# Performance work log

Hardware: AMD Instinct MI355X
Metric: run time of the kernel (lower is better)

## Reference

```python
import jax, jax.numpy as jnp
import numpy as np

N_EMBD = 1024
N_HEAD = 16
HEAD_DIM = N_EMBD // N_HEAD


def setup_inputs() -> dict:
    key = jax.random.key(0)
    ks = jax.random.split(key, 5)
    B, S = 2, 2048
    scale = 0.02
    return {
        "hidden_states": jax.random.normal(ks[0], (B, S, N_EMBD), dtype=jnp.float32),
        "w_attn": jax.random.normal(ks[1], (N_EMBD, 3 * N_EMBD), dtype=jnp.float32) * scale,
        "b_attn": jnp.zeros((3 * N_EMBD,), dtype=jnp.float32),
        "w_proj": jax.random.normal(ks[2], (N_EMBD, N_EMBD), dtype=jnp.float32) * scale,
        "b_proj": jnp.zeros((N_EMBD,), dtype=jnp.float32),
    }


def reference(hidden_states, w_attn, b_attn, w_proj, b_proj):
    B, S, _ = hidden_states.shape
    qkv = hidden_states @ w_attn + b_attn                     # [B,S,3E]
    q, k, v = jnp.split(qkv, 3, axis=-1)                      # each [B,S,E]

    def split_heads(t):  # [B,S,E] -> [B,H,S,D]
        return t.reshape(B, S, N_HEAD, HEAD_DIM).transpose(0, 2, 1, 3)

    q, k, v = split_heads(q), split_heads(k), split_heads(v)

    scores = jnp.einsum("bhqd,bhkd->bhqk", q, k) / np.sqrt(HEAD_DIM).astype(np.float32)
    causal = jnp.tril(jnp.ones((S, S), dtype=bool))
    scores = jnp.where(causal[None, None], scores, jnp.float32(-jnp.inf))
    attn = jax.nn.softmax(scores, axis=-1)                    # [B,H,S,S]
    out = jnp.einsum("bhqk,bhkd->bhqd", attn, v)              # [B,H,S,D]
    out = out.transpose(0, 2, 1, 3).reshape(B, S, N_EMBD)     # merge heads
    out = out @ w_proj + b_proj
    return out
```

## Files before the change

### kernel.cpp

```cpp
#include <hip/hip_runtime.h>
#include <hip/hip_bf16.h>


typedef __attribute__((ext_vector_type(4))) float  float4v;
typedef __attribute__((ext_vector_type(8))) short  short8v;
typedef __attribute__((ext_vector_type(4))) short  short4v;

#define ATT_SCALE 0.18033688011112042f

__device__ __forceinline__ short f2bf(float f) {
  union { float f; unsigned u; } v; v.f = f;
  unsigned r = v.u + 0x7fffu + ((v.u >> 16) & 1u);
  return (short)(r >> 16);
}
__device__ __forceinline__ float bf2f(short s) {
  union { unsigned u; float f; } v; v.u = ((unsigned)(unsigned short)s) << 16;
  return v.f;
}

__device__ __forceinline__ short4v pack_bf16x4(float a, float b, float c, float d) {
  unsigned x0 = __builtin_bit_cast(unsigned, a) + 0x8000u;
  unsigned x1 = __builtin_bit_cast(unsigned, b) + 0x8000u;
  unsigned x2 = __builtin_bit_cast(unsigned, c) + 0x8000u;
  unsigned x3 = __builtin_bit_cast(unsigned, d) + 0x8000u;
  union { unsigned u[2]; short4v s; } r;
  r.u[0] = __builtin_amdgcn_perm(x1, x0, 0x07060302);
  r.u[1] = __builtin_amdgcn_perm(x3, x2, 0x07060302);
  return r.s;
}

__device__ __forceinline__ short4v cvt_pk_bf16x4(float a, float b, float c, float d) {
  union { unsigned u[2]; short4v s; } r;
  asm("v_cvt_pk_bf16_f32 %0, %1, %2" : "=v"(r.u[0]) : "v"(a), "v"(b));
  asm("v_cvt_pk_bf16_f32 %0, %1, %2" : "=v"(r.u[1]) : "v"(c), "v"(d));
  return r.s;
}

__device__ __forceinline__ void gl_lds16(const void* g, void* l) {
  __builtin_amdgcn_global_load_lds(
      (const __attribute__((address_space(1))) unsigned*)g,
      (__attribute__((address_space(3))) unsigned*)l, 16, 0, 0);
}

__global__ __launch_bounds__(256) void prep_kernel(
    const float* __restrict__ hidden, const float* __restrict__ w_attn,
    const float* __restrict__ w_proj, short* __restrict__ hA,
    short* __restrict__ wqkvT, short* __restrict__ wprojT) {
  __shared__ float tile[32][33];
  const int bx = blockIdx.x, t = threadIdx.x;
  if (bx < 4096) {
    const size_t i = ((size_t)bx * 256 + t) * 4;
    float4v v = *(const float4v*)(hidden + i);
    short4v o;
    #pragma unroll
    for (int k = 0; k < 4; k++) o[k] = f2bf(v[k]);
    *(short4v*)(hA + i) = o;
    return;
  }
  const float* in; short* out; int R, C, cx, cy;
  if (bx < 4096 + 3072) {
    in = w_attn; out = wqkvT; R = 1024; C = 3072;
    cx = (bx - 4096) % 96; cy = (bx - 4096) / 96;
  } else {
    in = w_proj; out = wprojT; R = 1024; C = 1024;
    cx = (bx - 7168) % 32; cy = (bx - 7168) / 32;
  }
  const int tx = t & 31, ty = t >> 5;
  const int c0 = cx * 32, r0 = cy * 32;
  #pragma unroll
  for (int i = 0; i < 4; i++)
    tile[ty + i * 8][tx] = in[(size_t)(r0 + ty + i * 8) * C + c0 + tx];
  __syncthreads();
  #pragma unroll
  for (int i = 0; i < 4; i++) {
    const int cc = ty + i * 8;
    out[(size_t)(c0 + cc) * R + r0 + tx] = f2bf(tile[tx][cc]);
  }
}

__global__ __launch_bounds__(512, 2) void gemm_qkv256(
    const short* __restrict__ A, const short* __restrict__ Bt,
    const float* __restrict__ bias, short* __restrict__ qkv,
    short* __restrict__ vA)
{
  __shared__ short As[2][256][64];
  __shared__ short Bs[2][256][64];
  const int K = 1024;
  const int t = threadIdx.x;
  const int lane = t & 63, w = t >> 6;
  const int wm2 = w >> 2, wn4 = w & 3;
  const int l16 = lane & 15, quad = lane >> 4;
  const int e7 = l16 & 7;
  const int row0 = blockIdx.y * 256;
  const int col0 = blockIdx.x * 256;

  float4v acc[8][4] = {};

  const int srow = w * 8 + (lane >> 3);
  const int slog = (lane & 7) ^ (lane >> 3);
  const short* gA = A + (size_t)(row0 + srow) * K + slog * 8;
  const short* gB = Bt + (size_t)(col0 + srow) * K + slog * 8;
  const int sdst = (lane & 7) * 8;

  auto stageA = [&](int b, int qd, int kt) {
    gl_lds16(gA + (size_t)qd * 64 * K + kt * 64,
             &As[b][qd * 64 + w * 8 + (lane >> 3)][sdst]);
  };
  auto stageB = [&](int b, int qd, int kt) {
    gl_lds16(gB + (size_t)qd * 64 * K + kt * 64,
             &Bs[b][qd * 64 + w * 8 + (lane >> 3)][sdst]);
  };

  short8v af[4], bf0[4], bf1[4];
  auto ldA = [&](int b, int mh, int ks) {
    #pragma unroll
    for (int m = 0; m < 4; m++) {
      const int row = wm2 * 128 + mh * 64 + m * 16 + l16;
      af[m] = *(const short8v*)&As[b][row][((ks * 4 + quad) ^ e7) * 8];
    }
  };
  auto ldB = [&](short8v* bf, int b, int ks) {
    #pragma unroll
    for (int n = 0; n < 4; n++) {
      const int row = wn4 * 64 + n * 16 + l16;
      bf[n] = *(const short8v*)&Bs[b][row][((ks * 4 + quad) ^ e7) * 8];
    }
  };
  auto mm = [&](int mb, short8v* bf) {
    __builtin_amdgcn_s_setprio(1);
    #pragma unroll
    for (int m = 0; m < 4; m++)
      #pragma unroll
      for (int n = 0; n < 4; n++)
        acc[mb + m][n] =
            __builtin_amdgcn_mfma_f32_16x16x32_bf16(af[m], bf[n], acc[mb + m][n], 0, 0, 0);
    __builtin_amdgcn_s_setprio(0);
  };
  auto sync_mfma = [&]() {
    __builtin_amdgcn_sched_barrier(0);
    __builtin_amdgcn_s_barrier();
    asm volatile("s_waitcnt lgkmcnt(0)" ::: "memory");
    __builtin_amdgcn_sched_barrier(0);
  };
  auto endp = [&]() {
    __builtin_amdgcn_sched_barrier(0);
    __builtin_amdgcn_s_barrier();
    __builtin_amdgcn_sched_barrier(0);
  };

  #pragma unroll
  for (int qd = 0; qd < 4; qd++) stageA(0, qd, 0);
  #pragma unroll
  for (int qd = 0; qd < 4; qd++) stageB(0, qd, 0);
  #pragma unroll
  for (int qd = 0; qd < 4; qd++) stageB(1, qd, 1);
  asm volatile("s_waitcnt vmcnt(4)" ::: "memory");
  __builtin_amdgcn_s_barrier();
  __builtin_amdgcn_sched_barrier(0);

  const int NIT = K / 128;
  #pragma unroll 1
  for (int it = 0; it < NIT; it++) {
    const bool st = (it < NIT - 1);
    const int t1 = 2 * it + 1, t2 = 2 * it + 2, t3 = 2 * it + 3;

    ldA(0, 0, 0); ldB(bf0, 0, 0);
    stageA(1, 0, t1); stageA(1, 1, t1);
    sync_mfma(); mm(0, bf0); endp();
    ldA(0, 0, 1); ldB(bf1, 0, 1);
    stageA(1, 2, t1); stageA(1, 3, t1);
    sync_mfma(); mm(0, bf1); endp();
    ldA(0, 1, 0);
    if (st) { stageB(0, 0, t2); stageB(0, 1, t2); }
    sync_mfma(); mm(4, bf0); endp();
    ldA(0, 1, 1);
    if (st) { stageB(0, 2, t2); stageB(0, 3, t2); }
    if (st) asm volatile("s_waitcnt vmcnt(4)" ::: "memory");
    else    asm volatile("s_waitcnt vmcnt(0)" ::: "memory");
    sync_mfma(); mm(4, bf1); endp();

    ldA(1, 0, 0); ldB(bf0, 1, 0);
    if (st) { stageA(0, 0, t2); stageA(0, 1, t2); }
    sync_mfma(); mm(0, bf0); endp();
    ldA(1, 0, 1); ldB(bf1, 1, 1);
    if (st) { stageA(0, 2, t2); stageA(0, 3, t2); }
    sync_mfma(); mm(0, bf1); endp();
    ldA(1, 1, 0);
    if (st) { stageB(1, 0, t3); stageB(1, 1, t3); }
    sync_mfma(); mm(4, bf0); endp();
    ldA(1, 1, 1);
    if (st) { stageB(1, 2, t3); stageB(1, 3, t3); }
    if (st) asm volatile("s_waitcnt vmcnt(4)" ::: "memory");
    sync_mfma(); mm(4, bf1); endp();
  }

  if (col0 >= 2048) {
    const int b  = row0 >> 11;
    const int hh = ((col0 - 2048) >> 6) + wn4;
    #pragma unroll
    for (int ktl = 0; ktl < 2; ktl++) {
      const int kt = ((row0 & 2047) >> 6) + wm2 * 2 + ktl;
      short* vbase = vA + ((size_t)((b * 16 + hh) * 32 + kt) * 8) * 512;
      #pragma unroll
      for (int j = 0; j < 4; j++) {
        const float bv = bias[col0 + wn4 * 64 + j * 16 + l16];
        #pragma unroll
        for (int kwp = 0; kwp < 2; kwp++) {
          short8v s8;
          #pragma unroll
          for (int kw = 0; kw < 2; kw++) {
            const int mi = ktl * 4 + kwp * 2 + kw;
            short4v q4 = pack_bf16x4(acc[mi][j][0] + bv, acc[mi][j][1] + bv,
                                     acc[mi][j][2] + bv, acc[mi][j][3] + bv);
            #pragma unroll
            for (int r = 0; r < 4; r++) s8[kw * 4 + r] = q4[r];
          }
          *(short8v*)(vbase + ((size_t)(kwp * 4 + j) * 64 + lane) * 8) = s8;
        }
      }
    }
    return;
  }
  #pragma unroll
  for (int j = 0; j < 4; j++) {
    const int col = col0 + wn4 * 64 + j * 16 + l16;
    const float sc = (col < 1024) ? ATT_SCALE : 1.0f;
    const float bv = bias[col];
    #pragma unroll
    for (int mi = 0; mi < 8; mi++) {
      #pragma unroll
      for (int r = 0; r < 4; r++) {
        const int row = row0 + wm2 * 128 + mi * 16 + quad * 4 + r;
        qkv[(size_t)row * 3072 + col] = f2bf((acc[mi][j][r] + bv) * sc);
      }
    }
  }
}

__global__ __launch_bounds__(256, 2) void gemm_proj128(
    const short* __restrict__ A, const short* __restrict__ Bt,
    const float* __restrict__ bias, float* __restrict__ Cout)
{
  __shared__ short As[2][128][64];
  __shared__ short Bs[2][128][64];
  const int K = 1024;
  const int t = threadIdx.x;
  const int lane = t & 63, w = t >> 6;
  const int wm2 = w >> 1, wn2 = w & 1;
  const int l16 = lane & 15, quad = lane >> 4;
  const int e7 = l16 & 7;
  const int row0 = blockIdx.y * 128;
  const int col0 = blockIdx.x * 128;

  float4v acc[4][4] = {};

  const int srow = w * 8 + (lane >> 3);
  const int slog = (lane & 7) ^ (lane >> 3);
  const short* gA = A + (size_t)(row0 + srow) * K + slog * 8;
  const short* gB = Bt + (size_t)(col0 + srow) * K + slog * 8;
  const int sdst = (lane & 7) * 8;

  auto stageA = [&](int b, int qd, int kt) {
    gl_lds16(gA + (size_t)qd * 32 * K + kt * 64,
             &As[b][qd * 32 + w * 8 + (lane >> 3)][sdst]);
  };
  auto stageB = [&](int b, int qd, int kt) {
    gl_lds16(gB + (size_t)qd * 32 * K + kt * 64,
             &Bs[b][qd * 32 + w * 8 + (lane >> 3)][sdst]);
  };

  short8v af[2], bf0[4], bf1[4];
  auto ldA = [&](int b, int mh, int ks) {
    #pragma unroll
    for (int m = 0; m < 2; m++) {
      const int row = wm2 * 64 + mh * 32 + m * 16 + l16;
      af[m] = *(const short8v*)&As[b][row][((ks * 4 + quad) ^ e7) * 8];
    }
  };
  auto ldB = [&](short8v* bf, int b, int ks) {
    #pragma unroll
    for (int n = 0; n < 4; n++) {
      const int row = wn2 * 64 + n * 16 + l16;
      bf[n] = *(const short8v*)&Bs[b][row][((ks * 4 + quad) ^ e7) * 8];
    }
  };
  auto mm = [&](int mb, short8v* bf) {
    __builtin_amdgcn_s_setprio(1);
    #pragma unroll
    for (int m = 0; m < 2; m++)
      #pragma unroll
      for (int n = 0; n < 4; n++)
        acc[mb + m][n] =
            __builtin_amdgcn_mfma_f32_16x16x32_bf16(af[m], bf[n], acc[mb + m][n], 0, 0, 0);
    __builtin_amdgcn_s_setprio(0);
  };
  auto sync_mfma = [&]() {
    __builtin_amdgcn_sched_barrier(0);
    __builtin_amdgcn_s_barrier();
    asm volatile("s_waitcnt lgkmcnt(0)" ::: "memory");
    __builtin_amdgcn_sched_barrier(0);
  };
  auto endp = [&]() {
    __builtin_amdgcn_sched_barrier(0);
    __builtin_amdgcn_s_barrier();
    __builtin_amdgcn_sched_barrier(0);
  };

  #pragma unroll
  for (int qd = 0; qd < 4; qd++) stageA(0, qd, 0);
  #pragma unroll
  for (int qd = 0; qd < 4; qd++) stageB(0, qd, 0);
  #pragma unroll
  for (int qd = 0; qd < 4; qd++) stageB(1, qd, 1);
  asm volatile("s_waitcnt vmcnt(4)" ::: "memory");
  __builtin_amdgcn_s_barrier();
  __builtin_amdgcn_sched_barrier(0);

  const int NIT = K / 128;
  #pragma unroll 1
  for (int it = 0; it < NIT; it++) {
    const bool st = (it < NIT - 1);
    const int t1 = 2 * it + 1, t2 = 2 * it + 2, t3 = 2 * it + 3;

    ldA(0, 0, 0); ldB(bf0, 0, 0);
    stageA(1, 0, t1); stageA(1, 1, t1);
    sync_mfma(); mm(0, bf0); endp();
    ldA(0, 0, 1); ldB(bf1, 0, 1);
    stageA(1, 2, t1); stageA(1, 3, t1);
    sync_mfma(); mm(0, bf1); endp();
    ldA(0, 1, 0);
    if (st) { stageB(0, 0, t2); stageB(0, 1, t2); }
    sync_mfma(); mm(2, bf0); endp();
    ldA(0, 1, 1);
    if (st) { stageB(0, 2, t2); stageB(0, 3, t2); }
    if (st) asm volatile("s_waitcnt vmcnt(4)" ::: "memory");
    else    asm volatile("s_waitcnt vmcnt(0)" ::: "memory");
    sync_mfma(); mm(2, bf1); endp();

    ldA(1, 0, 0); ldB(bf0, 1, 0);
    if (st) { stageA(0, 0, t2); stageA(0, 1, t2); }
    sync_mfma(); mm(0, bf0); endp();
    ldA(1, 0, 1); ldB(bf1, 1, 1);
    if (st) { stageA(0, 2, t2); stageA(0, 3, t2); }
    sync_mfma(); mm(0, bf1); endp();
    ldA(1, 1, 0);
    if (st) { stageB(1, 0, t3); stageB(1, 1, t3); }
    sync_mfma(); mm(2, bf0); endp();
    ldA(1, 1, 1);
    if (st) { stageB(1, 2, t3); stageB(1, 3, t3); }
    if (st) asm volatile("s_waitcnt vmcnt(4)" ::: "memory");
    sync_mfma(); mm(2, bf1); endp();
  }

  #pragma unroll
  for (int j = 0; j < 4; j++) {
    const int col = col0 + wn2 * 64 + j * 16 + l16;
    const float bv = bias[col];
    #pragma unroll
    for (int mi = 0; mi < 4; mi++) {
      #pragma unroll
      for (int r = 0; r < 4; r++) {
        const int row = row0 + wm2 * 64 + mi * 16 + quad * 4 + r;
        Cout[(size_t)row * 1024 + col] = acc[mi][j][r] + bv;
      }
    }
  }
}

__global__ __launch_bounds__(128, 3) void attn_mfma(
    const short* __restrict__ qkv, const short* __restrict__ vA,
    short* __restrict__ P0, short* __restrict__ P1, float* __restrict__ lp)
{
  __shared__ short KA[2][8 * 512];

  const int bh = blockIdx.x;
  const int b = bh >> 4, h = bh & 15;
  const int s = 79 - blockIdx.y;
  int qt = 0, sbase = 0;
  for (;;) { const int nc = (qt >> 3) + 1; if (s < sbase + nc) break; sbase += nc; qt++; }
  const int c = s - sbase;
  const int kt0  = c * 8;
  const int kend = min(qt + 1, kt0 + 8);

  const int t = threadIdx.x;
  const int lane = t & 63, w = t >> 6;
  const int l16 = lane & 15, quad = lane >> 4;

  const size_t base = (size_t)b * 2048 * 3072;
  const int qoff = h * 64, koff = 1024 + h * 64;

  int qg[2];
  short8v qf[2][2];
  #pragma unroll
  for (int hh = 0; hh < 2; hh++) {
    qg[hh] = qt * 64 + w * 32 + hh * 16 + l16;
    #pragma unroll
    for (int ks = 0; ks < 2; ks++)
      qf[hh][ks] = *(const short8v*)(qkv + base + (size_t)qg[hh] * 3072
                                     + qoff + ks * 32 + quad * 8);
  }

  float4v O[2][4] = {};
  float l[2] = {0.0f, 0.0f};

  const short* kgw = qkv + base + (size_t)l16 * 3072 + koff + w * 32 + quad * 8;
  const short* vg  = vA + (size_t)(bh * 32) * 4096 + lane * 8;

  auto stageK = [&](int kt, int buf) {
    #pragma unroll
    for (int j = 0; j < 4; j++)
      gl_lds16(kgw + ((size_t)kt * 64 + j * 16) * 3072,
               &KA[buf][(w * 4 + j) * 512 + lane * 8]);
  };

  stageK(kt0, 0);

  for (int kt = kt0; kt < kend; kt++) {
    const int buf = (kt - kt0) & 1;
    __syncthreads();

    short8v vv[8];
    #pragma unroll
    for (int id = 0; id < 8; id++)
      vv[id] = *(const short8v*)(vg + (size_t)kt * 4096 + id * 512);

    if (kt + 1 < kend) stageK(kt + 1, buf ^ 1);

    float4v sv[2][4] = {};
    __builtin_amdgcn_s_setprio(1);
    #pragma unroll
    for (int ks = 0; ks < 2; ks++)
      #pragma unroll
      for (int jm = 0; jm < 4; jm++) {
        const short8v kf = *(const short8v*)&KA[buf][(ks * 4 + jm) * 512 + lane * 8];
        #pragma unroll
        for (int hh = 0; hh < 2; hh++)
          sv[hh][jm] = __builtin_amdgcn_mfma_f32_16x16x32_bf16(kf, qf[hh][ks],
                                                               sv[hh][jm], 0, 0, 0);
      }
    __builtin_amdgcn_s_setprio(0);

    if (kt == qt) {
      #pragma unroll
      for (int hh = 0; hh < 2; hh++)
        #pragma unroll
        for (int jm = 0; jm < 4; jm++) {
          const int kv = kt * 64 + jm * 16 + quad * 4;
          #pragma unroll
          for (int r = 0; r < 4; r++)
            if (kv + r > qg[hh]) sv[hh][jm][r] = -INFINITY;
        }
    }

    short4v pk[2][4];
    #pragma unroll
    for (int hh = 0; hh < 2; hh++)
      #pragma unroll
      for (int jm = 0; jm < 4; jm++) {
        float p0 = __builtin_amdgcn_exp2f(sv[hh][jm][0]);
        float p1 = __builtin_amdgcn_exp2f(sv[hh][jm][1]);
        float p2 = __builtin_amdgcn_exp2f(sv[hh][jm][2]);
        float p3 = __builtin_amdgcn_exp2f(sv[hh][jm][3]);
        l[hh] += (p0 + p1) + (p2 + p3);
        pk[hh][jm] = cvt_pk_bf16x4(p0, p1, p2, p3);
      }

    __builtin_amdgcn_s_setprio(1);
    #pragma unroll
    for (int id = 0; id < 8; id++) {
      const int kwp = id >> 2, dm = id & 3;
      const short8v v8 = vv[id];
      const short4v v0 = {v8[0], v8[1], v8[2], v8[3]};
      const short4v v1 = {v8[4], v8[5], v8[6], v8[7]};
      #pragma unroll
      for (int hh = 0; hh < 2; hh++) {
        O[hh][dm] = __builtin_amdgcn_mfma_f32_16x16x16bf16_1k(v0, pk[hh][kwp * 2],
                                                              O[hh][dm], 0, 0, 0);
        O[hh][dm] = __builtin_amdgcn_mfma_f32_16x16x16bf16_1k(v1, pk[hh][kwp * 2 + 1],
                                                              O[hh][dm], 0, 0, 0);
      }
    }
    __builtin_amdgcn_s_setprio(0);
  }

  #pragma unroll
  for (int hh = 0; hh < 2; hh++) {
    l[hh] += __shfl_xor(l[hh], 16);
    l[hh] += __shfl_xor(l[hh], 32);
  }
  const int i = bh * 80 + s;
  short* pp = (i < 2048) ? (P0 + (size_t)i * 4096) : (P1 + (size_t)(i - 2048) * 4096);
  #pragma unroll
  for (int hh = 0; hh < 2; hh++) {
    const int row = w * 32 + hh * 16 + l16;
    if (quad == 0) lp[(size_t)i * 64 + row] = l[hh];
    short* pr = pp + row * 64;
    #pragma unroll
    for (int dm = 0; dm < 4; dm++)
      *(short4v*)(pr + dm * 16 + quad * 4) =
          pack_bf16x4(O[hh][dm][0], O[hh][dm][1], O[hh][dm][2], O[hh][dm][3]);
  }
}

__global__ __launch_bounds__(256) void merge_attn(
    const short* __restrict__ P0, const short* __restrict__ P1,
    const float* __restrict__ lp, short* __restrict__ aout)
{
  const int idx = blockIdx.x * 256 + threadIdx.x;
  const int q = idx >> 7;
  const int rest = idx & 127;
  const int h  = rest >> 3;
  const int dg = (rest & 7) * 8;
  const int b  = q >> 11;
  const int qr = q & 2047;
  const int qt = qr >> 6;
  const int row = qr & 63;
  const int a = qt >> 3, bq = qt & 7;
  const int off = qt + 4 * a * (a - 1) + a * bq;
  const int nc  = a + 1;
  const int bh  = b * 16 + h;

  float acc[8] = {};
  float suml = 0.0f;
  for (int c = 0; c < nc; c++) {
    const int i = bh * 80 + off + c;
    const short* pp = (i < 2048) ? (P0 + (size_t)i * 4096) : (P1 + (size_t)(i - 2048) * 4096);
    const short8v o = *(const short8v*)(pp + row * 64 + dg);
    #pragma unroll
    for (int k = 0; k < 8; k++) acc[k] += bf2f(o[k]);
    suml += lp[(size_t)i * 64 + row];
  }
  const float inv = 1.0f / suml;
  short8v ov;
  #pragma unroll
  for (int k = 0; k < 8; k++) ov[k] = f2bf(acc[k] * inv);
  *(short8v*)(aout + (size_t)q * 1024 + h * 64 + dg) = ov;
}

extern "C" void kernel_launch(void* const* d_in, const int* in_sizes, int n_in,
                              void* d_out, int out_size, void* d_ws, size_t ws_size,
                              hipStream_t stream) {
  const float* hidden = (const float*)d_in[0];
  const float* w_attn = (const float*)d_in[1];
  const float* b_attn = (const float*)d_in[2];
  const float* w_proj = (const float*)d_in[3];
  const float* b_proj = (const float*)d_in[4];
  float* outp = (float*)d_out;

  char* ws = (char*)d_ws;
  short* hA     = (short*)(ws);
  float* lp     = (float*)(ws + 8ull  * 1024 * 1024);
  short* wqkvT  = (short*)(ws + 8ull  * 1024 * 1024);
  short* wprojT = (short*)(ws + 14ull * 1024 * 1024);
  short* qkvb   = (short*)(ws + 16ull * 1024 * 1024);
  short* vAbuf  = (short*)(ws + 40ull * 1024 * 1024);
  short* aout   = (short*)(ws + 40ull * 1024 * 1024);
  short* P0     = (short*)d_out;

  prep_kernel<<<8192, 256, 0, stream>>>(hidden, w_attn, w_proj, hA, wqkvT, wprojT);
  gemm_qkv256<<<dim3(12, 16), 512, 0, stream>>>(hA, wqkvT, b_attn, qkvb, vAbuf);
  attn_mfma<<<dim3(32, 80), 128, 0, stream>>>(qkvb, vAbuf, P0, hA, lp);
  merge_attn<<<2048, 256, 0, stream>>>(P0, hA, lp, aout);
  gemm_proj128<<<dim3(8, 32), 256, 0, stream>>>(aout, wprojT, b_proj, outp);
}
```

Measured before the change: 186.6 us.

## Use single-wave attention blocks loading K directly from global into registers

The attention kernel drops from two waves per block to one wave that handles all 64 query rows. K tiles are now read straight from global memory into registers instead of being staged through LDS with double buffering and __syncthreads. QK^T is computed one 16-key column group at a time so softmax can run interleaved with it. This removes the LDS traffic and block barriers, but raises register pressure (4x4 O accumulators plus K and V fragments) and lowers launch occupancy to 2. There is also no longer any prefetch of the next K tile.

Measured after the change: 188.1 us. No clear change (+0.8%).

```diff
diff --git a/kernel.cpp b/kernel.cpp
--- a/kernel.cpp
+++ b/kernel.cpp
@@ -367,12 +367,10 @@
   }
 }
 
-__global__ __launch_bounds__(128, 3) void attn_mfma(
+__global__ __launch_bounds__(64, 2) void attn_mfma(
     const short* __restrict__ qkv, const short* __restrict__ vA,
     short* __restrict__ P0, short* __restrict__ P1, float* __restrict__ lp)
 {
-  __shared__ short KA[2][8 * 512];
-
   const int bh = blockIdx.x;
   const int b = bh >> 4, h = bh & 15;
   const int s = 79 - blockIdx.y;
@@ -382,88 +380,74 @@
   const int kt0  = c * 8;
   const int kend = min(qt + 1, kt0 + 8);
 
-  const int t = threadIdx.x;
-  const int lane = t & 63, w = t >> 6;
+  const int lane = threadIdx.x & 63;
   const int l16 = lane & 15, quad = lane >> 4;
 
   const size_t base = (size_t)b * 2048 * 3072;
   const int qoff = h * 64, koff = 1024 + h * 64;
 
-  int qg[2];
-  short8v qf[2][2];
-  #pragma unroll
-  for (int hh = 0; hh < 2; hh++) {
-    qg[hh] = qt * 64 + w * 32 + hh * 16 + l16;
+  int qg[4];
+  short8v qf[4][2];
+  #pragma unroll
+  for (int hh = 0; hh < 4; hh++) {
+    qg[hh] = qt * 64 + hh * 16 + l16;
     #pragma unroll
     for (int ks = 0; ks < 2; ks++)
       qf[hh][ks] = *(const short8v*)(qkv + base + (size_t)qg[hh] * 3072
                                      + qoff + ks * 32 + quad * 8);
   }
 
-  float4v O[2][4] = {};
-  float l[2] = {0.0f, 0.0f};
-
-  const short* kgw = qkv + base + (size_t)l16 * 3072 + koff + w * 32 + quad * 8;
-  const short* vg  = vA + (size_t)(bh * 32) * 4096 + lane * 8;
-
-  auto stageK = [&](int kt, int buf) {
-    #pragma unroll
-    for (int j = 0; j < 4; j++)
-      gl_lds16(kgw + ((size_t)kt * 64 + j * 16) * 3072,
-               &KA[buf][(w * 4 + j) * 512 + lane * 8]);
-  };
-
-  stageK(kt0, 0);
+  float4v O[4][4] = {};
+  float l[4] = {0.0f, 0.0f, 0.0f, 0.0f};
+
+  const short* kg = qkv + base + (size_t)l16 * 3072 + koff + quad * 8;
+  const short* vg = vA + (size_t)(bh * 32) * 4096 + lane * 8;
 
   for (int kt = kt0; kt < kend; kt++) {
-    const int buf = (kt - kt0) & 1;
-    __syncthreads();
-
+    short8v kf[8];
+    #pragma unroll
+    for (int id = 0; id < 8; id++)
+      kf[id] = *(const short8v*)(kg + ((size_t)kt * 64 + (id & 3) * 16) * 3072
+                                    + (id >> 2) * 32);
     short8v vv[8];
     #pragma unroll
     for (int id = 0; id < 8; id++)
       vv[id] = *(const short8v*)(vg + (size_t)kt * 4096 + id * 512);
 
-    if (kt + 1 < kend) stageK(kt + 1, buf ^ 1);
-
-    float4v sv[2][4] = {};
-    __builtin_amdgcn_s_setprio(1);
-    #pragma unroll
-    for (int ks = 0; ks < 2; ks++)
-      #pragma unroll
-      for (int jm = 0; jm < 4; jm++) {
-        const short8v kf = *(const short8v*)&KA[buf][(ks * 4 + jm) * 512 + lane * 8];
+    short4v pk[4][4];
+    #pragma unroll
+    for (int jm = 0; jm < 4; jm++) {
+      float4v sv[4] = {};
+      __builtin_amdgcn_s_setprio(1);
+      #pragma unroll
+      for (int hh = 0; hh < 4; hh++)
+        sv[hh] = __builtin_amdgcn_mfma_f32_16x16x32_bf16(kf[jm], qf[hh][0],
+                                                         sv[hh], 0, 0, 0);
+      #pragma unroll
+      for (int hh = 0; hh < 4; hh++)
+        sv[hh] = __builtin_amdgcn_mfma_f32_16x16x32_bf16(kf[4 + jm], qf[hh][1],
+                                                         sv[hh], 0, 0, 0);
+      __builtin_amdgcn_s_setprio(0);
+
+      if (kt == qt) {
+        const int kv = kt * 64 + jm * 16 + quad * 4;
         #pragma unroll
-        for (int hh = 0; hh < 2; hh++)
-          sv[hh][jm] = __builtin_amdgcn_mfma_f32_16x16x32_bf16(kf, qf[hh][ks],
-                                                               sv[hh][jm], 0, 0, 0);
-      }
-    __builtin_amdgcn_s_setprio(0);
-
-    if (kt == qt) {
-      #pragma unroll
-      for (int hh = 0; hh < 2; hh++)
-        #pragma unroll
-        for (int jm = 0; jm < 4; jm++) {
-          const int kv = kt * 64 + jm * 16 + quad * 4;
+        for (int hh = 0; hh < 4; hh++)
           #pragma unroll
           for (int r = 0; r < 4; r++)
-            if (kv + r > qg[hh]) sv[hh][jm][r] = -INFINITY;
-        }
-    }
-
-    short4v pk[2][4];
-    #pragma unroll
-    for (int hh = 0; hh < 2; hh++)
-      #pragma unroll
-      for (int jm = 0; jm < 4; jm++) {
-        float p0 = __builtin_amdgcn_exp2f(sv[hh][jm][0]);
-        float p1 = __builtin_amdgcn_exp2f(sv[hh][jm][1]);
-        float p2 = __builtin_amdgcn_exp2f(sv[hh][jm][2]);
-        float p3 = __builtin_amdgcn_exp2f(sv[hh][jm][3]);
+            if (kv + r > qg[hh]) sv[hh][r] = -INFINITY;
+      }
+
+      #pragma unroll
+      for (int hh = 0; hh < 4; hh++) {
+        float p0 = __builtin_amdgcn_exp2f(sv[hh][0]);
+        float p1 = __builtin_amdgcn_exp2f(sv[hh][1]);
+        float p2 = __builtin_amdgcn_exp2f(sv[hh][2]);
+        float p3 = __builtin_amdgcn_exp2f(sv[hh][3]);
         l[hh] += (p0 + p1) + (p2 + p3);
         pk[hh][jm] = cvt_pk_bf16x4(p0, p1, p2, p3);
       }
+    }
 
     __builtin_amdgcn_s_setprio(1);
     #pragma unroll
@@ -473,7 +457,7 @@
       const short4v v0 = {v8[0], v8[1], v8[2], v8[3]};
       const short4v v1 = {v8[4], v8[5], v8[6], v8[7]};
       #pragma unroll
-      for (int hh = 0; hh < 2; hh++) {
+      for (int hh = 0; hh < 4; hh++) {
         O[hh][dm] = __builtin_amdgcn_mfma_f32_16x16x16bf16_1k(v0, pk[hh][kwp * 2],
                                                               O[hh][dm], 0, 0, 0);
         O[hh][dm] = __builtin_amdgcn_mfma_f32_16x16x16bf16_1k(v1, pk[hh][kwp * 2 + 1],
@@ -484,15 +468,15 @@
   }
 
   #pragma unroll
-  for (int hh = 0; hh < 2; hh++) {
+  for (int hh = 0; hh < 4; hh++) {
     l[hh] += __shfl_xor(l[hh], 16);
     l[hh] += __shfl_xor(l[hh], 32);
   }
   const int i = bh * 80 + s;
   short* pp = (i < 2048) ? (P0 + (size_t)i * 4096) : (P1 + (size_t)(i - 2048) * 4096);
   #pragma unroll
-  for (int hh = 0; hh < 2; hh++) {
-    const int row = w * 32 + hh * 16 + l16;
+  for (int hh = 0; hh < 4; hh++) {
+    const int row = hh * 16 + l16;
     if (quad == 0) lp[(size_t)i * 64 + row] = l[hh];
     short* pr = pp + row * 64;
     #pragma unroll
@@ -559,7 +543,7 @@
 
   prep_kernel<<<8192, 256, 0, stream>>>(hidden, w_attn, w_proj, hA, wqkvT, wprojT);
   gemm_qkv256<<<dim3(12, 16), 512, 0, stream>>>(hA, wqkvT, b_attn, qkvb, vAbuf);
-  attn_mfma<<<dim3(32, 80), 128, 0, stream>>>(qkvb, vAbuf, P0, hA, lp);
+  attn_mfma<<<dim3(32, 80), 64, 0, stream>>>(qkvb, vAbuf, P0, hA, lp);
   merge_attn<<<2048, 256, 0, stream>>>(P0, hA, lp, aout);
   gemm_proj128<<<dim3(8, 32), 256, 0, stream>>>(aout, wprojT, b_proj, outp);
 }
```
